# Optimization experiments

Measured on AMD Instinct MI355X. Metric: run time of the kernel, lower is better.

The kernel has to match this reference:

```python
import jax, jax.numpy as jnp
import numpy as np

HIDDEN = 2048
NUM_HEADS = 32
NUM_KV_HEADS = 8
HEAD_DIM = 64
ROPE_THETA = 10000.0


def _rope_tables(S, dtype=jnp.float32):
    freqs = 1.0 / (ROPE_THETA ** (jnp.arange(0, HEAD_DIM, 2, dtype=jnp.float32) / HEAD_DIM))
    angles = jnp.arange(S, dtype=jnp.float32)[:, None] * freqs[None, :]  # [S, D/2]
    return jnp.cos(angles).astype(dtype), jnp.sin(angles).astype(dtype)


def _apply_rope(x, cos, sin):
    # x: [B, H, S, D] with interleaved even/odd rotation pairs
    xe = x[..., 0::2]
    xo = x[..., 1::2]
    oe = xe * cos - xo * sin
    oo = xe * sin + xo * cos
    return jnp.stack([oe, oo], axis=-1).reshape(x.shape)


def setup_inputs() -> dict:
    key = jax.random.key(0)
    ks = jax.random.split(key, 5)
    scale = 0.02
    return {
        "x": jax.random.normal(ks[0], (2, 2048, HIDDEN), dtype=jnp.float32),
        "wq": jax.random.normal(ks[1], (NUM_HEADS * HEAD_DIM, HIDDEN), dtype=jnp.float32) * scale,
        "wk": jax.random.normal(ks[2], (NUM_KV_HEADS * HEAD_DIM, HIDDEN), dtype=jnp.float32) * scale,
        "wv": jax.random.normal(ks[3], (NUM_KV_HEADS * HEAD_DIM, HIDDEN), dtype=jnp.float32) * scale,
        "wo": jax.random.normal(ks[4], (HIDDEN, NUM_HEADS * HEAD_DIM), dtype=jnp.float32) * scale,
    }


def reference(x, wq, wk, wv, wo):
    B, S, _ = x.shape
    G = NUM_HEADS // NUM_KV_HEADS  # GQA group size

    q = (x @ wq.T).reshape(B, S, NUM_HEADS, HEAD_DIM).transpose(0, 2, 1, 3)      # [B,Hq,S,D]
    k = (x @ wk.T).reshape(B, S, NUM_KV_HEADS, HEAD_DIM).transpose(0, 2, 1, 3)   # [B,Hkv,S,D]
    v = (x @ wv.T).reshape(B, S, NUM_KV_HEADS, HEAD_DIM).transpose(0, 2, 1, 3)

    cos, sin = _rope_tables(S, x.dtype)
    q = _apply_rope(q, cos, sin)
    k = _apply_rope(k, cos, sin)

    # GQA without materializing repeated K/V: fold group dim into q
    qg = q.reshape(B, NUM_KV_HEADS, G, S, HEAD_DIM)
    scale = 1.0 / jnp.sqrt(jnp.asarray(HEAD_DIM, dtype=x.dtype))
    scores = jnp.einsum("bkgsd,bktd->bkgst", qg, k) * scale  # [B,Hkv,G,S,S]

    causal = jnp.tril(jnp.ones((S, S), dtype=bool))
    scores = jnp.where(causal, scores, jnp.finfo(scores.dtype).min)
    probs = jax.nn.softmax(scores, axis=-1)

    out = jnp.einsum("bkgst,bktd->bkgsd", probs, v)                 # [B,Hkv,G,S,D]
    out = out.reshape(B, NUM_HEADS, S, HEAD_DIM).transpose(0, 2, 1, 3).reshape(B, S, NUM_HEADS * HEAD_DIM)
    return out @ wo.T
```

## Files before the change

kernel.cpp:

```cpp
#include <hip/hip_runtime.h>
#include <hip/hip_bf16.h>

typedef __hip_bfloat16 bf16;
typedef __attribute__((ext_vector_type(8))) short short8;
typedef __attribute__((ext_vector_type(4))) float f32x4;

#define S_LEN 2048
#define BATCH 2
#define M_TOT 4096
#define HID 2048
#define NH 32
#define NKV 8
#define HD 64
#define KVD 512

#define MFMA16(a, b, c) __builtin_amdgcn_mfma_f32_16x16x32_bf16(a, b, c, 0, 0, 0)

__device__ __forceinline__ void gload_lds16(const bf16* g, bf16* l) {
    __builtin_amdgcn_global_load_lds((const __attribute__((address_space(1))) void*)g,
                                     (__attribute__((address_space(3))) void*)l,
                                     16, 0, 0);
}

__device__ __forceinline__ float b2f(short v) {
    unsigned u = ((unsigned)(unsigned short)v) << 16;
    float f; __builtin_memcpy(&f, &u, 4); return f;
}

#define N8_X   1048576
#define N8_WQ   524288
#define N8_WK   131072
#define N8_TOT 2359296
__global__ void cast_all_kernel(const float* __restrict__ x, const float* __restrict__ wq,
                                const float* __restrict__ wk, const float* __restrict__ wv,
                                const float* __restrict__ wo, bf16* __restrict__ dst) {
    int stride = gridDim.x * blockDim.x;
    for (int i = blockIdx.x * blockDim.x + threadIdx.x; i < N8_TOT; i += stride) {
        const float* s; int off;
        if (i < N8_X)                        { s = x;  off = i; }
        else if (i < N8_X + N8_WQ)           { s = wq; off = i - N8_X; }
        else if (i < N8_X + N8_WQ + N8_WK)   { s = wk; off = i - (N8_X + N8_WQ); }
        else if (i < N8_X + N8_WQ + 2*N8_WK) { s = wv; off = i - (N8_X + N8_WQ + N8_WK); }
        else                                 { s = wo; off = i - (N8_X + N8_WQ + 2*N8_WK); }
        const float4* sp = (const float4*)(s + (size_t)off * 8);
        float4 a = sp[0], b = sp[1];
        bf16 tmp[8];
        tmp[0] = __float2bfloat16(a.x); tmp[1] = __float2bfloat16(a.y);
        tmp[2] = __float2bfloat16(a.z); tmp[3] = __float2bfloat16(a.w);
        tmp[4] = __float2bfloat16(b.x); tmp[5] = __float2bfloat16(b.y);
        tmp[6] = __float2bfloat16(b.z); tmp[7] = __float2bfloat16(b.w);
        *(short8*)(dst + (size_t)i * 8) = *(short8*)tmp;
    }
}

__global__ void rope_tables_kernel(float* __restrict__ cosb, float* __restrict__ sinb) {
    int idx = blockIdx.x * blockDim.x + threadIdx.x;
    if (idx >= S_LEN * 32) return;
    int s = idx >> 5, d = idx & 31;
    float freq = powf(10000.0f, -(float)(2 * d) / 64.0f);
    float ang = (float)s * freq;
    cosb[idx] = cosf(ang);
    sinb[idx] = sinf(ang);
}

__device__ __forceinline__ short8 rope8(short8 v, float4 c, float4 s, float scale) {
    short8 o;
    const float* cp = (const float*)&c;
    const float* sp = (const float*)&s;
    #pragma unroll
    for (int m = 0; m < 4; m++) {
        float xe = b2f(v[2 * m]) * scale;
        float xo = b2f(v[2 * m + 1]) * scale;
        bf16 oe = __float2bfloat16(xe * cp[m] - xo * sp[m]);
        bf16 oo = __float2bfloat16(xe * sp[m] + xo * cp[m]);
        short se, so;
        __builtin_memcpy(&se, &oe, 2); __builtin_memcpy(&so, &oo, 2);
        o[2 * m] = se; o[2 * m + 1] = so;
    }
    return o;
}

__global__ void rope_k_kernel(bf16* __restrict__ buf, const float* __restrict__ cosb,
                              const float* __restrict__ sinb) {
    int idx = blockIdx.x * blockDim.x + threadIdx.x;
    if (idx >= M_TOT * 64) return;
    int m = idx >> 6, c = idx & 63;
    int e0 = c * 8;
    int d0 = (e0 & 63) >> 1;
    int s = m & (S_LEN - 1);
    bf16* p = buf + (size_t)m * KVD + e0;
    short8 v = *(const short8*)p;
    float4 cv = *(const float4*)(cosb + s * 32 + d0);
    float4 sv = *(const float4*)(sinb + s * 32 + d0);
    *(short8*)p = rope8(v, cv, sv, 1.0f);
}

__device__ __forceinline__ void gemm_core(const bf16* __restrict__ A,
                                          const bf16* __restrict__ W,
                                          int K, int m0, int n0,
                                          bf16* As, bf16* Bs,
                                          f32x4 acc[4][4]) {
    int tid = threadIdx.x;
    int lane = tid & 63, wid = tid >> 6;
    int wr = wid >> 1, wc = wid & 1;
    int lhi = lane >> 4, llo = lane & 15;
    int c0 = tid, c1 = tid + 256;
    int r0 = c0 >> 2, s0 = ((c0 & 3) ^ ((r0 >> 1) & 3)) * 8;
    int r1 = c1 >> 2, s1 = ((c1 & 3) ^ ((r1 >> 1) & 3)) * 8;
    const bf16* gA0 = A + (size_t)(m0 + r0) * K + s0;
    const bf16* gA1 = A + (size_t)(m0 + r1) * K + s1;
    const bf16* gB0 = W + (size_t)(n0 + r0) * K + s0;
    const bf16* gB1 = W + (size_t)(n0 + r1) * K + s1;

    auto stage = [&](int buf, int k0) {
        bf16* a = As + buf * 4096;
        bf16* b = Bs + buf * 4096;
        gload_lds16(gA0 + k0, a + c0 * 8);
        gload_lds16(gA1 + k0, a + c1 * 8);
        gload_lds16(gB0 + k0, b + c0 * 8);
        gload_lds16(gB1 + k0, b + c1 * 8);
    };
    auto compute = [&](int buf) {
        const bf16* Ac = As + buf * 4096;
        const bf16* Bc = Bs + buf * 4096;
        short8 af[4], bfr[4];
        #pragma unroll
        for (int i = 0; i < 4; i++) {
            int row = wr * 64 + i * 16 + llo;
            af[i] = *(const short8*)(Ac + row * 32 + ((lhi ^ ((row >> 1) & 3)) * 8));
        }
        #pragma unroll
        for (int j = 0; j < 4; j++) {
            int row = wc * 64 + j * 16 + llo;
            bfr[j] = *(const short8*)(Bc + row * 32 + ((lhi ^ ((row >> 1) & 3)) * 8));
        }
        #pragma unroll
        for (int i = 0; i < 4; i++)
            #pragma unroll
            for (int j = 0; j < 4; j++)
                acc[i][j] = MFMA16(af[i], bfr[j], acc[i][j]);
    };

    int nt = K / 32;
    stage(0, 0);
    stage(1, 32);
    int b0 = 0, b1 = 1, b2 = 2;
    for (int t = 0; t < nt - 1; ++t) {
        asm volatile("s_waitcnt vmcnt(4)" ::: "memory");
        __builtin_amdgcn_s_barrier();
        compute(b0);
        if (t + 2 < nt) stage(b2, (t + 2) * 32);
        int tmp = b0; b0 = b1; b1 = b2; b2 = tmp;
    }
    asm volatile("s_waitcnt vmcnt(0)" ::: "memory");
    __builtin_amdgcn_s_barrier();
    compute(b0);
}

__global__ __launch_bounds__(256) void gemm_qkv_kernel(
        const bf16* __restrict__ xb,
        const bf16* __restrict__ wq, const bf16* __restrict__ wk, const bf16* __restrict__ wv,
        bf16* __restrict__ qb, bf16* __restrict__ kb, bf16* __restrict__ vtb) {
    __shared__ bf16 As[3 * 128 * 32];
    __shared__ bf16 Bs[3 * 128 * 32];
    int by = blockIdx.y;
    const bf16* W; bf16* Cb; int n0, ldc, mode;
    if (by < 16)      { W = wq; Cb = qb;  n0 = by * 128;        ldc = 2048; mode = 0; }
    else if (by < 20) { W = wk; Cb = kb;  n0 = (by - 16) * 128; ldc = 512;  mode = 0; }
    else              { W = wv; Cb = vtb; n0 = (by - 20) * 128; ldc = 0;    mode = 1; }
    int bx = blockIdx.x;
    int bxs = (bx & 7) * 4 + (bx >> 3);
    int m0 = bxs * 128;

    f32x4 acc[4][4] = {};
    gemm_core(xb, W, HID, m0, n0, As, Bs, acc);

    int lane = threadIdx.x & 63, wid = threadIdx.x >> 6;
    int wr = wid >> 1, wc = wid & 1;
    int lhi = lane >> 4, llo = lane & 15;
    #pragma unroll
    for (int i = 0; i < 4; i++)
        #pragma unroll
        for (int j = 0; j < 4; j++) {
            int col = wc * 64 + j * 16 + llo;
            #pragma unroll
            for (int r = 0; r < 4; r++) {
                int row = wr * 64 + i * 16 + lhi * 4 + r;
                int m = m0 + row;
                float v = acc[i][j][r];
                if (mode == 0) {
                    Cb[(size_t)m * ldc + n0 + col] = __float2bfloat16(v);
                } else {
                    int bb = m >> 11, ss = m & 2047;
                    Cb[((size_t)(bb * 512 + n0 + col)) * S_LEN + ss] = __float2bfloat16(v);
                }
            }
        }
}

__global__ __launch_bounds__(256) void gemm_out_kernel(
        const bf16* __restrict__ attnb, const bf16* __restrict__ wob,
        float* __restrict__ out) {
    __shared__ bf16 As[3 * 128 * 32];
    __shared__ bf16 Bs[3 * 128 * 32];
    int bx = blockIdx.x;
    int bxs = (bx & 7) * 4 + (bx >> 3);
    int m0 = bxs * 128;
    int n0 = blockIdx.y * 128;
    f32x4 acc[4][4] = {};
    gemm_core(attnb, wob, HID, m0, n0, As, Bs, acc);

    int lane = threadIdx.x & 63, wid = threadIdx.x >> 6;
    int wr = wid >> 1, wc = wid & 1;
    int lhi = lane >> 4, llo = lane & 15;
    #pragma unroll
    for (int i = 0; i < 4; i++)
        #pragma unroll
        for (int j = 0; j < 4; j++) {
            int col = wc * 64 + j * 16 + llo;
            #pragma unroll
            for (int r = 0; r < 4; r++) {
                int row = wr * 64 + i * 16 + lhi * 4 + r;
                out[(size_t)(m0 + row) * HID + n0 + col] = acc[i][j][r];
            }
        }
}

__global__ __launch_bounds__(256, 4) void flash_kernel(
        const bf16* __restrict__ qb, const bf16* __restrict__ kb,
        const bf16* __restrict__ vtb, const float* __restrict__ cosb,
        const float* __restrict__ sinb, bf16* __restrict__ attnb) {
    __shared__ bf16 Ks[2][64 * 64];
    __shared__ bf16 Vs[2][64 * 64];
    __shared__ bf16 Pl[4][16 * 64];
    int bh = blockIdx.y;
    int b = bh >> 5, h = bh & 31;
    int kvh = h >> 2;
    int tid = threadIdx.x;
    int wid = tid >> 6, lane = tid & 63;
    int lhi = lane >> 4, llo = lane & 15;

    const bf16* Kg = kb + (size_t)(b * S_LEN) * KVD + kvh * HD;
    const bf16* Vg = vtb + (size_t)(b * 512 + kvh * 64) * S_LEN;

    int c0 = tid, c1 = tid + 256;
    int r0 = c0 >> 3, s0 = ((c0 & 7) ^ (r0 & 7)) * 8;
    int r1 = c1 >> 3, s1 = ((c1 & 7) ^ (r1 & 7)) * 8;

    bf16* pl = &Pl[wid][0];
    const int prd0 = llo * 64 + ((lhi ^ (llo & 7)) * 8);
    const int prd1 = llo * 64 + (((lhi + 4) ^ (llo & 7)) * 8);

    auto stage = [&](int buf, int t0) {
        gload_lds16(Kg + (size_t)(t0 + r0) * KVD + s0, &Ks[buf][c0 * 8]);
        gload_lds16(Kg + (size_t)(t0 + r1) * KVD + s1, &Ks[buf][c1 * 8]);
        gload_lds16(Vg + (size_t)r0 * S_LEN + t0 + s0, &Vs[buf][c0 * 8]);
        gload_lds16(Vg + (size_t)r1 * S_LEN + t0 + s1, &Vs[buf][c1 * 8]);
    };

    auto run_phase = [&](int j) {
        int qrow0 = j * 64 + wid * 16;
        int spos = qrow0 + llo;
        const bf16* qrow = qb + ((size_t)(b * S_LEN) + spos) * (NH * HD) + h * HD;
        float4 cv0 = *(const float4*)(cosb + spos * 32 + lhi * 4);
        float4 sv0 = *(const float4*)(sinb + spos * 32 + lhi * 4);
        float4 cv1 = *(const float4*)(cosb + spos * 32 + 16 + lhi * 4);
        float4 sv1 = *(const float4*)(sinb + spos * 32 + 16 + lhi * 4);
        short8 qf0 = rope8(*(const short8*)(qrow + lhi * 8), cv0, sv0, 0.125f);
        short8 qf1 = rope8(*(const short8*)(qrow + 32 + lhi * 8), cv1, sv1, 0.125f);

        f32x4 acc[4] = {};
        float psum[4] = {0.f, 0.f, 0.f, 0.f};

        stage(0, 0);
        asm volatile("s_waitcnt vmcnt(0)" ::: "memory");
        __builtin_amdgcn_s_barrier();
        int cur = 0;
        for (int t = 0; t <= j; ++t) {
            int t0 = t * 64;
            if (t < j) stage(cur ^ 1, t0 + 64);
            const bf16* Kc = &Ks[cur][0];
            const bf16* Vc = &Vs[cur][0];
            f32x4 z[4];
            #pragma unroll
            for (int cb = 0; cb < 4; cb++) {
                int row = cb * 16 + llo;
                int x = row & 7;
                short8 k0 = *(const short8*)(Kc + row * 64 + ((lhi ^ x) * 8));
                short8 k1 = *(const short8*)(Kc + row * 64 + (((lhi + 4) ^ x) * 8));
                f32x4 zz = {0.f, 0.f, 0.f, 0.f};
                zz = MFMA16(qf0, k0, zz);
                zz = MFMA16(qf1, k1, zz);
                z[cb] = zz;
            }
            if (t == j) {
                #pragma unroll
                for (int cb = 0; cb < 4; cb++)
                    #pragma unroll
                    for (int r = 0; r < 4; r++) {
                        float p = __expf(z[cb][r]);
                        p = (t0 + cb * 16 + llo <= qrow0 + lhi * 4 + r) ? p : 0.f;
                        psum[r] += p;
                        int row = lhi * 4 + r;
                        pl[row * 64 + (((2 * cb + (llo >> 3)) ^ (row & 7)) * 8) + (llo & 7)]
                            = __float2bfloat16(p);
                    }
            } else {
                #pragma unroll
                for (int cb = 0; cb < 4; cb++)
                    #pragma unroll
                    for (int r = 0; r < 4; r++) {
                        float p = __expf(z[cb][r]);
                        psum[r] += p;
                        int row = lhi * 4 + r;
                        pl[row * 64 + (((2 * cb + (llo >> 3)) ^ (row & 7)) * 8) + (llo & 7)]
                            = __float2bfloat16(p);
                    }
            }
            short8 pa0 = *(const short8*)(pl + prd0);
            short8 pa1 = *(const short8*)(pl + prd1);
            #pragma unroll
            for (int jb = 0; jb < 4; jb++) {
                int row = jb * 16 + llo;
                int x = row & 7;
                short8 v0 = *(const short8*)(Vc + row * 64 + ((lhi ^ x) * 8));
                short8 v1 = *(const short8*)(Vc + row * 64 + (((lhi + 4) ^ x) * 8));
                acc[jb] = MFMA16(pa0, v0, acc[jb]);
                acc[jb] = MFMA16(pa1, v1, acc[jb]);
            }
            asm volatile("s_waitcnt vmcnt(0)" ::: "memory");
            __builtin_amdgcn_s_barrier();
            cur ^= 1;
        }
        #pragma unroll
        for (int off = 1; off < 16; off <<= 1)
            #pragma unroll
            for (int r = 0; r < 4; r++)
                psum[r] += __shfl_xor(psum[r], off, 64);
        float inv[4];
        #pragma unroll
        for (int r = 0; r < 4; r++) inv[r] = 1.0f / psum[r];
        size_t obase = ((size_t)(b * S_LEN) + qrow0) * (NH * HD) + h * HD;
        #pragma unroll
        for (int jb = 0; jb < 4; jb++)
            #pragma unroll
            for (int r = 0; r < 4; r++)
                attnb[obase + (size_t)(lhi * 4 + r) * (NH * HD) + jb * 16 + llo] =
                    __float2bfloat16(acc[jb][r] * inv[r]);
    };

    run_phase(blockIdx.x);
    run_phase(31 - blockIdx.x);
}

extern "C" void kernel_launch(void* const* d_in, const int* in_sizes, int n_in,
                              void* d_out, int out_size, void* d_ws, size_t ws_size,
                              hipStream_t stream) {
    const float* x  = (const float*)d_in[0];
    const float* wq = (const float*)d_in[1];
    const float* wk = (const float*)d_in[2];
    const float* wv = (const float*)d_in[3];
    const float* wo = (const float*)d_in[4];
    float* out = (float*)d_out;

    char* ws = (char*)d_ws;
    size_t off = 0;
    auto alloc = [&](size_t bytes) { void* p = ws + off; off += (bytes + 255) & ~(size_t)255; return p; };
    bf16* xb   = (bf16*)alloc((size_t)M_TOT * HID * 2);
    bf16* wqb  = (bf16*)alloc((size_t)HID * HID * 2);
    bf16* wkb  = (bf16*)alloc((size_t)512 * HID * 2);
    bf16* wvb  = (bf16*)alloc((size_t)512 * HID * 2);
    bf16* wob  = (bf16*)alloc((size_t)HID * HID * 2);
    bf16* qb   = (bf16*)alloc((size_t)M_TOT * 2048 * 2);
    bf16* kb   = (bf16*)alloc((size_t)M_TOT * 512 * 2);
    bf16* vtb  = (bf16*)alloc((size_t)M_TOT * 512 * 2);
    bf16* attnb= (bf16*)alloc((size_t)M_TOT * 2048 * 2);
    float* cosb= (float*)alloc((size_t)S_LEN * 32 * 4);
    float* sinb= (float*)alloc((size_t)S_LEN * 32 * 4);

    cast_all_kernel<<<2048, 256, 0, stream>>>(x, wq, wk, wv, wo, xb);

    rope_tables_kernel<<<(S_LEN * 32 + 255) / 256, 256, 0, stream>>>(cosb, sinb);

    gemm_qkv_kernel<<<dim3(M_TOT / 128, 24), 256, 0, stream>>>(xb, wqb, wkb, wvb, qb, kb, vtb);

    rope_k_kernel<<<(M_TOT * 64 + 255) / 256, 256, 0, stream>>>(kb, cosb, sinb);

    flash_kernel<<<dim3(16, BATCH * NH), 256, 0, stream>>>(qb, kb, vtb, cosb, sinb, attnb);

    gemm_out_kernel<<<dim3(M_TOT / 128, HID / 128), 256, 0, stream>>>(attnb, wob, out);
}
```

Before: 198.3 us.

## Transpose QK^T MFMA so each lane owns one query row; packed bf16 P stores

Swaps the MFMA operand order so the score tile is transposed and each lane holds four consecutive keys for a single query row. This lets P be written to LDS as packed bf16 pairs via v_cvt_pk_bf16_f32 with 8-byte stores and a new swizzle, and lets the row sum stay in one scalar per lane. The per-row shuffle reduction shrinks to two xor shuffles plus a broadcast. It also folds log2(e) into the Q scale so exp2f replaces __expf, and branches only on the mask instead of duplicating the loop body. The changed LDS swizzle and index mapping carry correctness risk.

```diff
diff --git a/kernel.cpp b/kernel.cpp
--- a/kernel.cpp
+++ b/kernel.cpp
@@ -13,6 +13,7 @@
 #define NKV 8
 #define HD 64
 #define KVD 512
+#define QSCALE 0.180336880f
 
 #define MFMA16(a, b, c) __builtin_amdgcn_mfma_f32_16x16x32_bf16(a, b, c, 0, 0, 0)
 
@@ -25,6 +26,12 @@
 __device__ __forceinline__ float b2f(short v) {
     unsigned u = ((unsigned)(unsigned short)v) << 16;
     float f; __builtin_memcpy(&f, &u, 4); return f;
+}
+
+__device__ __forceinline__ unsigned pk_bf16(float lo, float hi) {
+    unsigned d;
+    asm("v_cvt_pk_bf16_f32 %0, %1, %2" : "=v"(d) : "v"(lo), "v"(hi));
+    return d;
 }
 
 #define N8_X   1048576
@@ -248,8 +255,11 @@
     int r1 = c1 >> 3, s1 = ((c1 & 7) ^ (r1 & 7)) * 8;
 
     bf16* pl = &Pl[wid][0];
-    const int prd0 = llo * 64 + ((lhi ^ (llo & 7)) * 8);
-    const int prd1 = llo * 64 + (((lhi + 4) ^ (llo & 7)) * 8);
+    int e = llo & 14;
+    bf16* pw = pl + llo * 64 + (lhi ^ (e & 3)) * 4;
+    const int ehi = e >> 2;
+    const int prd0 = llo * 64 + (((lhi * 2) ^ e) * 4);
+    const int prd1 = llo * 64 + (((8 + lhi * 2) ^ e) * 4);
 
     auto stage = [&](int buf, int t0) {
         gload_lds16(Kg + (size_t)(t0 + r0) * KVD + s0, &Ks[buf][c0 * 8]);
@@ -266,11 +276,12 @@
         float4 sv0 = *(const float4*)(sinb + spos * 32 + lhi * 4);
         float4 cv1 = *(const float4*)(cosb + spos * 32 + 16 + lhi * 4);
         float4 sv1 = *(const float4*)(sinb + spos * 32 + 16 + lhi * 4);
-        short8 qf0 = rope8(*(const short8*)(qrow + lhi * 8), cv0, sv0, 0.125f);
-        short8 qf1 = rope8(*(const short8*)(qrow + 32 + lhi * 8), cv1, sv1, 0.125f);
+        short8 qf0 = rope8(*(const short8*)(qrow + lhi * 8), cv0, sv0, QSCALE);
+        short8 qf1 = rope8(*(const short8*)(qrow + 32 + lhi * 8), cv1, sv1, QSCALE);
 
         f32x4 acc[4] = {};
-        float psum[4] = {0.f, 0.f, 0.f, 0.f};
+        float psum = 0.f;
+        int qloc = wid * 16 + llo;
 
         stage(0, 0);
         asm volatile("s_waitcnt vmcnt(0)" ::: "memory");
@@ -281,48 +292,43 @@
             if (t < j) stage(cur ^ 1, t0 + 64);
             const bf16* Kc = &Ks[cur][0];
             const bf16* Vc = &Vs[cur][0];
+            int x = llo & 7;
             f32x4 z[4];
             #pragma unroll
             for (int cb = 0; cb < 4; cb++) {
                 int row = cb * 16 + llo;
-                int x = row & 7;
                 short8 k0 = *(const short8*)(Kc + row * 64 + ((lhi ^ x) * 8));
                 short8 k1 = *(const short8*)(Kc + row * 64 + (((lhi + 4) ^ x) * 8));
                 f32x4 zz = {0.f, 0.f, 0.f, 0.f};
-                zz = MFMA16(qf0, k0, zz);
-                zz = MFMA16(qf1, k1, zz);
+                zz = MFMA16(k0, qf0, zz);
+                zz = MFMA16(k1, qf1, zz);
                 z[cb] = zz;
             }
-            if (t == j) {
-                #pragma unroll
-                for (int cb = 0; cb < 4; cb++)
-                    #pragma unroll
-                    for (int r = 0; r < 4; r++) {
-                        float p = __expf(z[cb][r]);
-                        p = (t0 + cb * 16 + llo <= qrow0 + lhi * 4 + r) ? p : 0.f;
-                        psum[r] += p;
-                        int row = lhi * 4 + r;
-                        pl[row * 64 + (((2 * cb + (llo >> 3)) ^ (row & 7)) * 8) + (llo & 7)]
-                            = __float2bfloat16(p);
-                    }
-            } else {
-                #pragma unroll
-                for (int cb = 0; cb < 4; cb++)
-                    #pragma unroll
-                    for (int r = 0; r < 4; r++) {
-                        float p = __expf(z[cb][r]);
-                        psum[r] += p;
-                        int row = lhi * 4 + r;
-                        pl[row * 64 + (((2 * cb + (llo >> 3)) ^ (row & 7)) * 8) + (llo & 7)]
-                            = __float2bfloat16(p);
-                    }
+            bool diag = (t == j);
+            #pragma unroll
+            for (int cb = 0; cb < 4; cb++) {
+                float p0 = exp2f(z[cb][0]);
+                float p1 = exp2f(z[cb][1]);
+                float p2 = exp2f(z[cb][2]);
+                float p3 = exp2f(z[cb][3]);
+                if (diag) {
+                    int kl = cb * 16 + lhi * 4;
+                    p0 = (kl + 0 <= qloc) ? p0 : 0.f;
+                    p1 = (kl + 1 <= qloc) ? p1 : 0.f;
+                    p2 = (kl + 2 <= qloc) ? p2 : 0.f;
+                    p3 = (kl + 3 <= qloc) ? p3 : 0.f;
+                }
+                psum += (p0 + p1) + (p2 + p3);
+                uint2 w;
+                w.x = pk_bf16(p0, p1);
+                w.y = pk_bf16(p2, p3);
+                *(uint2*)(pw + 16 * (cb ^ ehi)) = w;
             }
             short8 pa0 = *(const short8*)(pl + prd0);
             short8 pa1 = *(const short8*)(pl + prd1);
             #pragma unroll
             for (int jb = 0; jb < 4; jb++) {
                 int row = jb * 16 + llo;
-                int x = row & 7;
                 short8 v0 = *(const short8*)(Vc + row * 64 + ((lhi ^ x) * 8));
                 short8 v1 = *(const short8*)(Vc + row * 64 + (((lhi + 4) ^ x) * 8));
                 acc[jb] = MFMA16(pa0, v0, acc[jb]);
@@ -332,14 +338,12 @@
             __builtin_amdgcn_s_barrier();
             cur ^= 1;
         }
-        #pragma unroll
-        for (int off = 1; off < 16; off <<= 1)
-            #pragma unroll
-            for (int r = 0; r < 4; r++)
-                psum[r] += __shfl_xor(psum[r], off, 64);
+        psum += __shfl_xor(psum, 16, 64);
+        psum += __shfl_xor(psum, 32, 64);
         float inv[4];
         #pragma unroll
-        for (int r = 0; r < 4; r++) inv[r] = 1.0f / psum[r];
+        for (int r = 0; r < 4; r++)
+            inv[r] = 1.0f / __shfl(psum, lhi * 4 + r, 64);
         size_t obase = ((size_t)(b * S_LEN) + qrow0) * (NH * HD) + h * HD;
         #pragma unroll
         for (int jb = 0; jb < 4; jb++)
```

Result: no change. 201.5 us (+1.6%).
